# Optimization experiments

Measured on AMD Instinct MI355X. Metric: run time of the kernel, lower is better.

The kernel has to match this reference:

```python
import jax, jax.numpy as jnp
import numpy as np

B = 32768
K = 4096  # num_embeddings
D = 512   # embedding_dim
COMMITMENT_COST = 0.25


def setup_inputs() -> dict:
    key = jax.random.key(0)
    k1, k2 = jax.random.split(key)
    inputs = jax.random.normal(k1, (B, D), dtype=jnp.float32)
    # nn.Embedding weight init: uniform(-1/K, 1/K)
    codebook = jax.random.uniform(k2, (K, D), dtype=jnp.float32,
                                  minval=-1.0 / K, maxval=1.0 / K)
    return {"inputs": inputs, "codebook": codebook}


def reference(inputs, codebook):
    distances = (jnp.sum(inputs ** 2, axis=1, keepdims=True)
                 + jnp.sum(codebook ** 2, axis=1)
                 - 2.0 * jnp.matmul(inputs, codebook.T))
    encoding_indices = jnp.argmin(distances, axis=1)  # [B]
    # one-hot encodings are part of the module's returned dict
    encodings = jax.nn.one_hot(encoding_indices, K, dtype=inputs.dtype)  # [B, K]
    # quantized = encodings @ codebook == direct gather (same math)
    quantized = codebook[encoding_indices]  # [B, D]

    sg = jax.lax.stop_gradient
    e_latent_loss = jnp.mean((sg(quantized) - inputs) ** 2)
    q_latent_loss = jnp.mean((quantized - sg(inputs)) ** 2)
    loss = q_latent_loss + COMMITMENT_COST * e_latent_loss

    # straight-through estimator
    quantized_st = inputs + sg(quantized - inputs)

    avg_probs = jnp.mean(encodings, axis=0)  # [K]
    perplexity = jnp.exp(-jnp.sum(avg_probs * jnp.log(avg_probs + 1e-10)))

    return quantized_st, encoding_indices, loss, perplexity, encodings
```

## Files before the change

kernel.cpp:

```cpp
#include <hip/hip_runtime.h>
#include <hip/hip_bf16.h>


typedef __attribute__((ext_vector_type(8))) short bf16x8;
typedef __attribute__((ext_vector_type(4))) float f32x4;

#define BB 32768
#define KK 4096
#define DD 512

#define IDX_OFF  (BB*DD)
#define LOSS_OFF (IDX_OFF + BB)
#define PERP_OFF (LOSS_OFF + 1)
#define ENC_OFF  (PERP_OFF + 1)

#define WSB_XSQ  0
#define WSB_ESQ  131072
#define WSB_IDX  147456
#define WSB_HIST 278528
#define WSB_LOSS 294912
#define WSB_EBF2 294928
#define WSB_XBF  4489232
#define WSB_PART 38043664

#define MARG 2.5e-4f
#define NCAND 16

static __device__ __forceinline__ unsigned short f2bf(float f) {
    __hip_bfloat16 h = __float2bfloat16(f);
    return *reinterpret_cast<unsigned short*>(&h);
}

static __device__ __forceinline__ unsigned int packscore(float s, int col) {
    unsigned int u = __float_as_uint(s);
    u ^= (u & 0x80000000u) ? 0xFFFFFFFFu : 0x80000000u;
    return (u & 0xFFFFF000u) | (unsigned int)col;
}
static __device__ __forceinline__ float unpackscore(unsigned int p) {
    unsigned int u = p & 0xFFFFF000u;
    u = (u & 0x80000000u) ? (u ^ 0x80000000u) : ~u;
    return __uint_as_float(u);
}

static __device__ __forceinline__ void gll16(const void* g, void* l) {
    __builtin_amdgcn_global_load_lds(
        (const __attribute__((address_space(1))) unsigned int*)g,
        (__attribute__((address_space(3))) unsigned int*)l, 16, 0, 0);
}

__global__ __launch_bounds__(256) void init_kernel(int* __restrict__ hist,
                                                   double* __restrict__ loss_acc) {
    int i = blockIdx.x * 256 + threadIdx.x;
    if (i < KK) hist[i] = 0;
    if (i == 0) *loss_acc = 0.0;
}

__global__ __launch_bounds__(256) void npsum_kernel(const float* __restrict__ X,
                                                    const float* __restrict__ E,
                                                    float* __restrict__ xsq,
                                                    float* __restrict__ esq) {
    __shared__ float sq[4][512];
    __shared__ float ub[4][64];
    __shared__ float bb[4][4];
    int w = threadIdx.x >> 6, lane = threadIdx.x & 63;
    int row = blockIdx.x * 4 + w;
    const float* src; float* dst;
    if (row < BB) { src = X + (size_t)row * DD;        dst = xsq + row; }
    else          { src = E + (size_t)(row - BB) * DD; dst = esq + (row - BB); }
    #pragma unroll
    for (int m = 0; m < 8; ++m) {
        float v = src[m * 64 + lane];
        sq[w][m * 64 + lane] = __fmul_rn(v, v);
    }
    __syncthreads();
    {
        int b = lane >> 4, l = lane & 15;
        const float* s = &sq[w][b * 128];
        float t = __fadd_rn(
            __fadd_rn(__fadd_rn(s[l], s[16 + l]), __fadd_rn(s[32 + l], s[48 + l])),
            __fadd_rn(__fadd_rn(s[64 + l], s[80 + l]), __fadd_rn(s[96 + l], s[112 + l])));
        ub[w][lane] = t;
    }
    __syncthreads();
    if (lane < 4) {
        const float* u = &ub[w][lane * 16];
        float T3[8], T6[4];
        #pragma unroll
        for (int i = 0; i < 8; ++i) T3[i] = __fadd_rn(u[i], u[i + 8]);
        #pragma unroll
        for (int i = 0; i < 4; ++i) T6[i] = __fadd_rn(T3[i], T3[i + 4]);
        bb[w][lane] = __fadd_rn(__fadd_rn(T6[0], T6[2]), __fadd_rn(T6[1], T6[3]));
    }
    __syncthreads();
    if (lane == 0)
        *dst = __fadd_rn(__fadd_rn(bb[w][0], bb[w][1]), __fadd_rn(bb[w][2], bb[w][3]));
}

__global__ __launch_bounds__(256) void pack_kernel(const float* __restrict__ src,
                                                   unsigned short* __restrict__ dst) {
    int t = blockIdx.x * 256 + threadIdx.x;
    int chunk = t >> 10, u = t & 1023;
    int rb = chunk >> 3, kt = chunk & 7;
    int nf = u >> 7, ks = (u >> 6) & 1, lane = u & 63;
    int row = rb * 128 + nf * 16 + (lane & 15);
    int k   = kt * 64 + ks * 32 + (lane >> 4) * 8;
    const float4* s = (const float4*)(src + (size_t)row * DD + k);
    float4 a = s[0], b = s[1];
    union { bf16x8 v; unsigned short us[8]; } pk;
    pk.us[0] = f2bf(a.x); pk.us[1] = f2bf(a.y); pk.us[2] = f2bf(a.z); pk.us[3] = f2bf(a.w);
    pk.us[4] = f2bf(b.x); pk.us[5] = f2bf(b.y); pk.us[6] = f2bf(b.z); pk.us[7] = f2bf(b.w);
    *(bf16x8*)(dst + (size_t)t * 8) = pk.v;
}

__global__ __launch_bounds__(256, 2) void gemm_screen(
    const unsigned short* __restrict__ Xbf, const unsigned short* __restrict__ Ebf2,
    const float* __restrict__ esqw, uint2* __restrict__ partials)
{
    __shared__ __align__(16) char pool[65536];

    const int tid = threadIdx.x;
    const int w = tid >> 6, lane = tid & 63;
    const int c = lane & 15, g = lane >> 4;
    const int bid = blockIdx.x;
    const int orig = (bid & 7) * 1024 + (bid >> 3);
    const int rb = orig >> 5, cb = orig & 31;
    const int row0 = rb * 128, col0 = cb * 128;
    const int mw = w >> 1, nw = w & 1;

    const char* Xc = (const char*)Xbf  + (size_t)rb * 8 * 16384;
    const char* Ec = (const char*)Ebf2 + (size_t)cb * 8 * 16384;

    f32x4 acc[4][4];
    #pragma unroll
    for (int i = 0; i < 4; ++i)
        #pragma unroll
        for (int j = 0; j < 4; ++j) acc[i][j] = (f32x4){0.f, 0.f, 0.f, 0.f};

    #define STAGE(srcc_, kt_, dstoff_) { \
        const char* s_ = (srcc_) + (size_t)(kt_) * 16384 + (size_t)tid * 16; \
        char* d_ = pool + (dstoff_) + w * 1024; \
        gll16(s_,         d_); \
        gll16(s_ + 4096,  d_ + 4096); \
        gll16(s_ + 8192,  d_ + 8192); \
        gll16(s_ + 12288, d_ + 12288); }

    STAGE(Xc, 0, 0); STAGE(Ec, 0, 32768);
    __syncthreads();
    int buf = 0;
    for (int kt = 0; kt < 8; ++kt) {
        if (kt < 7) {
            STAGE(Xc, kt + 1, (buf ^ 1) * 16384);
            STAGE(Ec, kt + 1, 32768 + (buf ^ 1) * 16384);
        }
        const char* Ap = pool + buf * 16384;
        const char* Bp = pool + 32768 + buf * 16384;
        #pragma unroll
        for (int ks = 0; ks < 2; ++ks) {
            bf16x8 af[4], bfr[4];
            #pragma unroll
            for (int i = 0; i < 4; ++i) {
                af[i]  = *(const bf16x8*)(Ap + ((((mw * 4 + i) * 2 + ks) * 64) + lane) * 16);
                bfr[i] = *(const bf16x8*)(Bp + ((((nw * 4 + i) * 2 + ks) * 64) + lane) * 16);
            }
            #pragma unroll
            for (int mf = 0; mf < 4; ++mf)
                #pragma unroll
                for (int nf = 0; nf < 4; ++nf)
                    acc[mf][nf] = __builtin_amdgcn_mfma_f32_16x16x32_bf16(af[mf], bfr[nf], acc[mf][nf], 0, 0, 0);
        }
        __syncthreads();
        buf ^= 1;
    }

    uint2* P = (uint2*)pool;
    #pragma unroll
    for (int mf = 0; mf < 4; ++mf) {
        #pragma unroll
        for (int r = 0; r < 4; ++r) {
            unsigned int q1 = 0xFFFFFFFFu, q2 = 0xFFFFFFFFu;
            int rowl = mw * 64 + mf * 16 + g * 4 + r;
            #pragma unroll
            for (int nf = 0; nf < 4; ++nf) {
                int col = col0 + nw * 64 + nf * 16 + c;
                float s = fmaf(-2.0f, acc[mf][nf][r], esqw[col]);
                unsigned int q = packscore(s, col);
                if (q < q1) { q2 = q1; q1 = q; } else if (q < q2) q2 = q;
            }
            P[(nw * 128 + rowl) * 16 + c] = make_uint2(q1, q2);
        }
    }
    __syncthreads();
    if (tid < 128) {
        int row = tid;
        #pragma unroll
        for (int n2 = 0; n2 < 2; ++n2) {
            unsigned int m1 = 0xFFFFFFFFu, m2 = 0xFFFFFFFFu;
            #pragma unroll 4
            for (int cc = 0; cc < 16; ++cc) {
                uint2 e = P[(n2 * 128 + row) * 16 + cc];
                if (e.x < m1) { m2 = m1; m1 = e.x; } else if (e.x < m2) m2 = e.x;
                if (e.y < m1) { m2 = m1; m1 = e.y; } else if (e.y < m2) m2 = e.y;
            }
            partials[(size_t)(cb * 2 + n2) * BB + row0 + row] = make_uint2(m1, m2);
        }
    }
    #undef STAGE
}

__global__ __launch_bounds__(256) void reduce_kernel(
    const float* __restrict__ X, const float* __restrict__ E,
    const float* __restrict__ xsqw, const float* __restrict__ esqw,
    const uint2* __restrict__ partials, int* __restrict__ idxbuf,
    int* __restrict__ hist, double* __restrict__ loss_acc,
    float* __restrict__ out)
{
    __shared__ double lred[256];
    const int row = blockIdx.x * 256 + threadIdx.x;
    unsigned int m = 0xFFFFFFFFu;
    for (int e = 0; e < 64; ++e) m = min(m, partials[(size_t)e * BB + row].x);
    float lim = unpackscore(m) + MARG;
    int cand[NCAND]; int nc = 0;
    for (int e = 0; e < 64; ++e) {
        uint2 p = partials[(size_t)e * BB + row];
        if (unpackscore(p.x) <= lim && nc < NCAND) cand[nc++] = (int)(p.x & 0xFFFu);
        if (unpackscore(p.y) <= lim && nc < NCAND) cand[nc++] = (int)(p.y & 0xFFFu);
    }
    const float* xr = X + (size_t)row * DD;
    float xs = xsqw[row];
    float bd = 3.0e38f; int bk = 0x7fffffff;
    for (int cidx = 0; cidx < nc; ++cidx) {
        int k = cand[cidx] & (KK - 1);
        const float* er = E + (size_t)k * DD;
        float q1 = 0.f, q2 = 0.f;
        for (int d = 0; d < 384; ++d)   q1 = fmaf(xr[d], er[d], q1);
        for (int d = 384; d < 512; ++d) q2 = fmaf(xr[d], er[d], q2);
        float dot = __fadd_rn(q1, q2);
        float t1  = __fadd_rn(xs, esqw[k]);
        float dnp = __fsub_rn(t1, __fmul_rn(2.0f, dot));
        if (dnp < bd || (dnp == bd && k < bk)) { bd = dnp; bk = k; }
    }
    const float* er = E + (size_t)bk * DD;
    double ls = 0.0;
    for (int d = 0; d < DD; ++d) {
        double df = (double)xr[d] - (double)er[d];
        ls = fma(df, df, ls);
    }
    idxbuf[row] = bk;
    out[IDX_OFF + row] = (float)bk;
    atomicAdd(&hist[bk], 1);
    lred[threadIdx.x] = ls;
    __syncthreads();
    for (int t = 128; t > 0; t >>= 1) {
        if (threadIdx.x < t) lred[threadIdx.x] += lred[threadIdx.x + t];
        __syncthreads();
    }
    if (threadIdx.x == 0) atomicAdd(loss_acc, lred[0]);
}

__global__ __launch_bounds__(256) void encq_kernel(const int* __restrict__ idxbuf,
                                                   const float* __restrict__ E,
                                                   float* __restrict__ out) {
    int row = blockIdx.x;
    int idx = idxbuf[row];
    ((float2*)out)[(size_t)row * 256 + threadIdx.x] =
        ((const float2*)E)[(size_t)idx * 256 + threadIdx.x];
    float2* erow = (float2*)(out + ENC_OFF) + (size_t)row * (KK / 2);
    int half = idx >> 1;
    float2 one;
    if (idx & 1) { one.x = 0.f; one.y = 1.f; } else { one.x = 1.f; one.y = 0.f; }
    float2 z; z.x = 0.f; z.y = 0.f;
    for (int c = threadIdx.x; c < KK / 2; c += 256)
        erow[c] = (c == half) ? one : z;
}

__global__ __launch_bounds__(256) void fin_kernel(const int* __restrict__ hist,
                                                  const double* __restrict__ loss_acc,
                                                  float* __restrict__ out) {
    __shared__ double red[256];
    int tid = threadIdx.x;
    double s = 0.0;
    for (int k = tid; k < KK; k += 256) {
        double p = (double)hist[k] * (1.0 / 32768.0);
        s += p * log(p + 1e-10);
    }
    red[tid] = s;
    __syncthreads();
    for (int t = 128; t > 0; t >>= 1) {
        if (tid < t) red[tid] += red[tid + t];
        __syncthreads();
    }
    if (tid == 0) {
        double perp = exp(-red[0]);
        double L = loss_acc[0] * (1.0 / ((double)BB * (double)DD));
        out[LOSS_OFF] = (float)(1.25 * L);
        out[PERP_OFF] = (float)perp;
    }
}

extern "C" void kernel_launch(void* const* d_in, const int* in_sizes, int n_in,
                              void* d_out, int out_size, void* d_ws, size_t ws_size,
                              hipStream_t stream) {
    const float* X; const float* E;
    if (in_sizes[0] == BB * DD) { X = (const float*)d_in[0]; E = (const float*)d_in[1]; }
    else                        { X = (const float*)d_in[1]; E = (const float*)d_in[0]; }
    float* out = (float*)d_out;

    float* xsq = (float*)((char*)d_ws + WSB_XSQ);
    float* esq = (float*)((char*)d_ws + WSB_ESQ);
    int* idxbuf = (int*)((char*)d_ws + WSB_IDX);
    int* hist   = (int*)((char*)d_ws + WSB_HIST);
    double* loss_acc = (double*)((char*)d_ws + WSB_LOSS);
    unsigned short* Ebf2 = (unsigned short*)((char*)d_ws + WSB_EBF2);
    unsigned short* Xbf  = (unsigned short*)((char*)d_ws + WSB_XBF);
    uint2* partials = (uint2*)((char*)d_ws + WSB_PART);

    hipLaunchKernelGGL(init_kernel, dim3(16), dim3(256), 0, stream, hist, loss_acc);
    hipLaunchKernelGGL(npsum_kernel, dim3((BB + KK) / 4), dim3(256), 0, stream,
                       X, E, xsq, esq);
    hipLaunchKernelGGL(pack_kernel, dim3(1024), dim3(256), 0, stream, E, Ebf2);
    hipLaunchKernelGGL(pack_kernel, dim3(8192), dim3(256), 0, stream, X, Xbf);
    hipLaunchKernelGGL(gemm_screen, dim3(8192), dim3(256), 0, stream,
                       Xbf, Ebf2, esq, partials);
    hipLaunchKernelGGL(reduce_kernel, dim3(BB / 256), dim3(256), 0, stream,
                       X, E, xsq, esq, partials, idxbuf, hist, loss_acc, out);
    hipLaunchKernelGGL(encq_kernel, dim3(BB), dim3(256), 0, stream, idxbuf, E, out);
    hipLaunchKernelGGL(fin_kernel, dim3(1), dim3(256), 0, stream, hist, loss_acc, out);
}
```

Before: 477.2 us.

## Enlarge GEMM screen tile to 256x256 with 512 threads and shuffle-based top-2

Grows the bf16 MFMA screening tile from 128x128 to 256x256 and the block from 256 to 512 threads (8 waves each holding 8x4 accumulator fragments), so each staged byte of X and codebook is reused twice as often. The pack kernel layout changes to match 256-row chunks. The per-row top-2 is merged across lanes with xor shuffles instead of an LDS scratch pass, and the esq values are hoisted into registers. The cost is 128KB of dynamic LDS per block, which with launch_bounds(512,2) may not fit two blocks per CU and may raise register pressure. The reduce kernel still reads 64 partials per row, which stays consistent because the count becomes 16 column blocks times 4 waves.

```diff
diff --git a/kernel.cpp b/kernel.cpp
--- a/kernel.cpp
+++ b/kernel.cpp
@@ -99,10 +99,10 @@
 __global__ __launch_bounds__(256) void pack_kernel(const float* __restrict__ src,
                                                    unsigned short* __restrict__ dst) {
     int t = blockIdx.x * 256 + threadIdx.x;
-    int chunk = t >> 10, u = t & 1023;
-    int rb = chunk >> 3, kt = chunk & 7;
-    int nf = u >> 7, ks = (u >> 6) & 1, lane = u & 63;
-    int row = rb * 128 + nf * 16 + (lane & 15);
+    int chunk = t >> 11, u = t & 2047;
+    int rb2 = chunk >> 3, kt = chunk & 7;
+    int rf = u >> 7, ks = (u >> 6) & 1, lane = u & 63;
+    int row = rb2 * 256 + rf * 16 + (lane & 15);
     int k   = kt * 64 + ks * 32 + (lane >> 4) * 8;
     const float4* s = (const float4*)(src + (size_t)row * DD + k);
     float4 a = s[0], b = s[1];
@@ -112,96 +112,93 @@
     *(bf16x8*)(dst + (size_t)t * 8) = pk.v;
 }
 
-__global__ __launch_bounds__(256, 2) void gemm_screen(
+__global__ __launch_bounds__(512, 2) void gemm_screen(
     const unsigned short* __restrict__ Xbf, const unsigned short* __restrict__ Ebf2,
     const float* __restrict__ esqw, uint2* __restrict__ partials)
 {
-    __shared__ __align__(16) char pool[65536];
+    extern __shared__ __align__(16) char pool[];
 
     const int tid = threadIdx.x;
     const int w = tid >> 6, lane = tid & 63;
     const int c = lane & 15, g = lane >> 4;
     const int bid = blockIdx.x;
-    const int orig = (bid & 7) * 1024 + (bid >> 3);
-    const int rb = orig >> 5, cb = orig & 31;
-    const int row0 = rb * 128, col0 = cb * 128;
-    const int mw = w >> 1, nw = w & 1;
-
-    const char* Xc = (const char*)Xbf  + (size_t)rb * 8 * 16384;
-    const char* Ec = (const char*)Ebf2 + (size_t)cb * 8 * 16384;
-
-    f32x4 acc[4][4];
+    const int orig = (bid & 7) * 256 + (bid >> 3);
+    const int rb2 = orig >> 4, cb2 = orig & 15;
+    const int row0 = rb2 * 256, col0 = cb2 * 256;
+    const int mw = w >> 2, nw = w & 3;
+
+    const char* Xc = (const char*)Xbf  + (size_t)rb2 * 8 * 32768;
+    const char* Ec = (const char*)Ebf2 + (size_t)cb2 * 8 * 32768;
+
+    f32x4 acc[8][4];
     #pragma unroll
-    for (int i = 0; i < 4; ++i)
+    for (int i = 0; i < 8; ++i)
         #pragma unroll
         for (int j = 0; j < 4; ++j) acc[i][j] = (f32x4){0.f, 0.f, 0.f, 0.f};
 
     #define STAGE(srcc_, kt_, dstoff_) { \
-        const char* s_ = (srcc_) + (size_t)(kt_) * 16384 + (size_t)tid * 16; \
+        const char* s_ = (srcc_) + (size_t)(kt_) * 32768 + (size_t)tid * 16; \
         char* d_ = pool + (dstoff_) + w * 1024; \
-        gll16(s_,         d_); \
-        gll16(s_ + 4096,  d_ + 4096); \
-        gll16(s_ + 8192,  d_ + 8192); \
-        gll16(s_ + 12288, d_ + 12288); }
-
-    STAGE(Xc, 0, 0); STAGE(Ec, 0, 32768);
+        gll16(s_,          d_); \
+        gll16(s_ + 8192,   d_ + 8192); \
+        gll16(s_ + 16384,  d_ + 16384); \
+        gll16(s_ + 24576,  d_ + 24576); }
+
+    STAGE(Xc, 0, 0); STAGE(Ec, 0, 65536);
     __syncthreads();
     int buf = 0;
     for (int kt = 0; kt < 8; ++kt) {
         if (kt < 7) {
-            STAGE(Xc, kt + 1, (buf ^ 1) * 16384);
-            STAGE(Ec, kt + 1, 32768 + (buf ^ 1) * 16384);
+            STAGE(Xc, kt + 1, (buf ^ 1) * 32768);
+            STAGE(Ec, kt + 1, 65536 + (buf ^ 1) * 32768);
         }
-        const char* Ap = pool + buf * 16384;
-        const char* Bp = pool + 32768 + buf * 16384;
+        const char* Ap = pool + buf * 32768;
+        const char* Bp = pool + 65536 + buf * 32768;
         #pragma unroll
         for (int ks = 0; ks < 2; ++ks) {
-            bf16x8 af[4], bfr[4];
+            bf16x8 bfr[4];
             #pragma unroll
-            for (int i = 0; i < 4; ++i) {
-                af[i]  = *(const bf16x8*)(Ap + ((((mw * 4 + i) * 2 + ks) * 64) + lane) * 16);
-                bfr[i] = *(const bf16x8*)(Bp + ((((nw * 4 + i) * 2 + ks) * 64) + lane) * 16);
+            for (int j = 0; j < 4; ++j)
+                bfr[j] = *(const bf16x8*)(Bp + ((((nw * 4 + j) * 2 + ks) * 64) + lane) * 16);
+            #pragma unroll
+            for (int i = 0; i < 8; ++i) {
+                bf16x8 af = *(const bf16x8*)(Ap + ((((mw * 8 + i) * 2 + ks) * 64) + lane) * 16);
+                #pragma unroll
+                for (int j = 0; j < 4; ++j)
+                    acc[i][j] = __builtin_amdgcn_mfma_f32_16x16x32_bf16(af, bfr[j], acc[i][j], 0, 0, 0);
             }
-            #pragma unroll
-            for (int mf = 0; mf < 4; ++mf)
-                #pragma unroll
-                for (int nf = 0; nf < 4; ++nf)
-                    acc[mf][nf] = __builtin_amdgcn_mfma_f32_16x16x32_bf16(af[mf], bfr[nf], acc[mf][nf], 0, 0, 0);
         }
         __syncthreads();
         buf ^= 1;
     }
 
-    uint2* P = (uint2*)pool;
+    float es[4];
     #pragma unroll
-    for (int mf = 0; mf < 4; ++mf) {
+    for (int nf = 0; nf < 4; ++nf) es[nf] = esqw[col0 + nw * 64 + nf * 16 + c];
+    #pragma unroll
+    for (int mf = 0; mf < 8; ++mf) {
         #pragma unroll
         for (int r = 0; r < 4; ++r) {
             unsigned int q1 = 0xFFFFFFFFu, q2 = 0xFFFFFFFFu;
-            int rowl = mw * 64 + mf * 16 + g * 4 + r;
             #pragma unroll
             for (int nf = 0; nf < 4; ++nf) {
                 int col = col0 + nw * 64 + nf * 16 + c;
-                float s = fmaf(-2.0f, acc[mf][nf][r], esqw[col]);
+                float s = fmaf(-2.0f, acc[mf][nf][r], es[nf]);
                 unsigned int q = packscore(s, col);
                 if (q < q1) { q2 = q1; q1 = q; } else if (q < q2) q2 = q;
             }
-            P[(nw * 128 + rowl) * 16 + c] = make_uint2(q1, q2);
-        }
-    }
-    __syncthreads();
-    if (tid < 128) {
-        int row = tid;
-        #pragma unroll
-        for (int n2 = 0; n2 < 2; ++n2) {
-            unsigned int m1 = 0xFFFFFFFFu, m2 = 0xFFFFFFFFu;
-            #pragma unroll 4
-            for (int cc = 0; cc < 16; ++cc) {
-                uint2 e = P[(n2 * 128 + row) * 16 + cc];
-                if (e.x < m1) { m2 = m1; m1 = e.x; } else if (e.x < m2) m2 = e.x;
-                if (e.y < m1) { m2 = m1; m1 = e.y; } else if (e.y < m2) m2 = e.y;
+            #pragma unroll
+            for (int off = 1; off < 16; off <<= 1) {
+                unsigned int o1 = (unsigned int)__shfl_xor((int)q1, off, 64);
+                unsigned int o2 = (unsigned int)__shfl_xor((int)q2, off, 64);
+                unsigned int n1 = min(q1, o1);
+                unsigned int n2 = min(max(q1, o1), min(q2, o2));
+                q1 = n1; q2 = n2;
             }
-            partials[(size_t)(cb * 2 + n2) * BB + row0 + row] = make_uint2(m1, m2);
+            if (c == 0) {
+                int row = row0 + mw * 128 + mf * 16 + g * 4 + r;
+                partials[(size_t)(cb2 * 4 + nw) * BB + row] = make_uint2(q1, q2);
+            }
         }
     }
     #undef STAGE
@@ -319,7 +316,7 @@
                        X, E, xsq, esq);
     hipLaunchKernelGGL(pack_kernel, dim3(1024), dim3(256), 0, stream, E, Ebf2);
     hipLaunchKernelGGL(pack_kernel, dim3(8192), dim3(256), 0, stream, X, Xbf);
-    hipLaunchKernelGGL(gemm_screen, dim3(8192), dim3(256), 0, stream,
+    hipLaunchKernelGGL(gemm_screen, dim3(2048), dim3(512), 131072, stream,
                        Xbf, Ebf2, esq, partials);
     hipLaunchKernelGGL(reduce_kernel, dim3(BB / 256), dim3(256), 0, stream,
                        X, E, xsq, esq, partials, idxbuf, hist, loss_acc, out);
```

New measurement: 489.4 us. +2.6%, slower.

## Fuse X bf16 packing into norm kernel and halve GEMM LDS tiles

Applied to the files above, without the earlier changes.

The separate X pack pass is merged into the squared-norm kernel, so X is read from global memory once, and the row sum of squares now uses vectorized float4 loads. The bf16 tile layout changes to 256-row groups with 32-wide k-steps. The GEMM now stages 32-wide k slices over 16 iterations instead of 64-wide over 8, which halves LDS use so launch bounds can ask for 4 blocks per CU. The cost is twice as many barriers and smaller load batches per iteration. The fp32 summation order for the norms is changed, which could shift rounding slightly.

```diff
diff --git a/kernel.cpp b/kernel.cpp
--- a/kernel.cpp
+++ b/kernel.cpp
@@ -55,27 +55,44 @@
     if (i == 0) *loss_acc = 0.0;
 }
 
-__global__ __launch_bounds__(256) void npsum_kernel(const float* __restrict__ X,
-                                                    const float* __restrict__ E,
-                                                    float* __restrict__ xsq,
-                                                    float* __restrict__ esq) {
+__global__ __launch_bounds__(256) void npsum_pack_kernel(const float* __restrict__ X,
+                                                         const float* __restrict__ E,
+                                                         float* __restrict__ xsq,
+                                                         float* __restrict__ esq,
+                                                         unsigned short* __restrict__ Xbf) {
     __shared__ float sq[4][512];
     __shared__ float ub[4][64];
     __shared__ float bb[4][4];
     int w = threadIdx.x >> 6, lane = threadIdx.x & 63;
     int row = blockIdx.x * 4 + w;
     const float* src; float* dst;
-    if (row < BB) { src = X + (size_t)row * DD;        dst = xsq + row; }
-    else          { src = E + (size_t)(row - BB) * DD; dst = esq + (row - BB); }
-    #pragma unroll
-    for (int m = 0; m < 8; ++m) {
-        float v = src[m * 64 + lane];
-        sq[w][m * 64 + lane] = __fmul_rn(v, v);
+    bool isx = (row < BB);
+    if (isx) { src = X + (size_t)row * DD;        dst = xsq + row; }
+    else     { src = E + (size_t)(row - BB) * DD; dst = esq + (row - BB); }
+    const float4* s4 = (const float4*)(src + lane * 8);
+    float4 a = s4[0], b = s4[1];
+    sq[w][lane * 8 + 0] = __fmul_rn(a.x, a.x);
+    sq[w][lane * 8 + 1] = __fmul_rn(a.y, a.y);
+    sq[w][lane * 8 + 2] = __fmul_rn(a.z, a.z);
+    sq[w][lane * 8 + 3] = __fmul_rn(a.w, a.w);
+    sq[w][lane * 8 + 4] = __fmul_rn(b.x, b.x);
+    sq[w][lane * 8 + 5] = __fmul_rn(b.y, b.y);
+    sq[w][lane * 8 + 6] = __fmul_rn(b.z, b.z);
+    sq[w][lane * 8 + 7] = __fmul_rn(b.w, b.w);
+    if (isx) {
+        int kt64 = lane >> 3, ks = (lane >> 2) & 1, oct = lane & 3;
+        int rf = (row >> 4) & 15;
+        size_t unit = ((size_t)((row >> 8) * 8 + kt64)) * 2048
+                    + (size_t)((rf * 2 + ks) * 64 + oct * 16 + (row & 15));
+        union { bf16x8 v; unsigned short us[8]; } pk;
+        pk.us[0] = f2bf(a.x); pk.us[1] = f2bf(a.y); pk.us[2] = f2bf(a.z); pk.us[3] = f2bf(a.w);
+        pk.us[4] = f2bf(b.x); pk.us[5] = f2bf(b.y); pk.us[6] = f2bf(b.z); pk.us[7] = f2bf(b.w);
+        *(bf16x8*)(Xbf + unit * 8) = pk.v;
     }
     __syncthreads();
     {
-        int b = lane >> 4, l = lane & 15;
-        const float* s = &sq[w][b * 128];
+        int b2 = lane >> 4, l = lane & 15;
+        const float* s = &sq[w][b2 * 128];
         float t = __fadd_rn(
             __fadd_rn(__fadd_rn(s[l], s[16 + l]), __fadd_rn(s[32 + l], s[48 + l])),
             __fadd_rn(__fadd_rn(s[64 + l], s[80 + l]), __fadd_rn(s[96 + l], s[112 + l])));
@@ -96,13 +113,13 @@
         *dst = __fadd_rn(__fadd_rn(bb[w][0], bb[w][1]), __fadd_rn(bb[w][2], bb[w][3]));
 }
 
-__global__ __launch_bounds__(256) void pack_kernel(const float* __restrict__ src,
-                                                   unsigned short* __restrict__ dst) {
+__global__ __launch_bounds__(256) void packE_kernel(const float* __restrict__ src,
+                                                    unsigned short* __restrict__ dst) {
     int t = blockIdx.x * 256 + threadIdx.x;
-    int chunk = t >> 10, u = t & 1023;
-    int rb = chunk >> 3, kt = chunk & 7;
-    int nf = u >> 7, ks = (u >> 6) & 1, lane = u & 63;
-    int row = rb * 128 + nf * 16 + (lane & 15);
+    int chunk = t >> 11, u = t & 2047;
+    int rb2 = chunk >> 3, kt = chunk & 7;
+    int rf = u >> 7, ks = (u >> 6) & 1, lane = u & 63;
+    int row = rb2 * 256 + rf * 16 + (lane & 15);
     int k   = kt * 64 + ks * 32 + (lane >> 4) * 8;
     const float4* s = (const float4*)(src + (size_t)row * DD + k);
     float4 a = s[0], b = s[1];
@@ -112,11 +129,11 @@
     *(bf16x8*)(dst + (size_t)t * 8) = pk.v;
 }
 
-__global__ __launch_bounds__(256, 2) void gemm_screen(
+__global__ __launch_bounds__(256, 4) void gemm_screen(
     const unsigned short* __restrict__ Xbf, const unsigned short* __restrict__ Ebf2,
     const float* __restrict__ esqw, uint2* __restrict__ partials)
 {
-    __shared__ __align__(16) char pool[65536];
+    __shared__ __align__(16) char pool[32768];
 
     const int tid = threadIdx.x;
     const int w = tid >> 6, lane = tid & 63;
@@ -127,8 +144,9 @@
     const int row0 = rb * 128, col0 = cb * 128;
     const int mw = w >> 1, nw = w & 1;
 
-    const char* Xc = (const char*)Xbf  + (size_t)rb * 8 * 16384;
-    const char* Ec = (const char*)Ebf2 + (size_t)cb * 8 * 16384;
+    const int hA = rb & 1, hB = cb & 1;
+    const char* Xc = (const char*)Xbf  + (size_t)(rb >> 1) * 8 * 32768;
+    const char* Ec = (const char*)Ebf2 + (size_t)(cb >> 1) * 8 * 32768;
 
     f32x4 acc[4][4];
     #pragma unroll
@@ -136,38 +154,35 @@
         #pragma unroll
         for (int j = 0; j < 4; ++j) acc[i][j] = (f32x4){0.f, 0.f, 0.f, 0.f};
 
-    #define STAGE(srcc_, kt_, dstoff_) { \
-        const char* s_ = (srcc_) + (size_t)(kt_) * 16384 + (size_t)tid * 16; \
-        char* d_ = pool + (dstoff_) + w * 1024; \
-        gll16(s_,         d_); \
-        gll16(s_ + 4096,  d_ + 4096); \
-        gll16(s_ + 8192,  d_ + 8192); \
-        gll16(s_ + 12288, d_ + 12288); }
-
-    STAGE(Xc, 0, 0); STAGE(Ec, 0, 32768);
+    #define STAGE(srcc_, h_, kt_, dstoff_) { \
+        const char* sb_ = (srcc_) + (size_t)((kt_) >> 1) * 32768; \
+        const int ks_ = (kt_) & 1; \
+        _Pragma("unroll") for (int it_ = 0; it_ < 2; ++it_) { \
+            const char* s_ = sb_ + (size_t)((((h_) * 8 + it_ * 4 + w) * 2 + ks_) * 64 + lane) * 16; \
+            char* d_ = pool + (dstoff_) + (it_ * 4 + w) * 1024; \
+            gll16(s_, d_); } }
+
+    STAGE(Xc, hA, 0, 0); STAGE(Ec, hB, 0, 16384);
     __syncthreads();
     int buf = 0;
-    for (int kt = 0; kt < 8; ++kt) {
-        if (kt < 7) {
-            STAGE(Xc, kt + 1, (buf ^ 1) * 16384);
-            STAGE(Ec, kt + 1, 32768 + (buf ^ 1) * 16384);
+    for (int kt = 0; kt < 16; ++kt) {
+        if (kt < 15) {
+            STAGE(Xc, hA, kt + 1, (buf ^ 1) * 8192);
+            STAGE(Ec, hB, kt + 1, 16384 + (buf ^ 1) * 8192);
         }
-        const char* Ap = pool + buf * 16384;
-        const char* Bp = pool + 32768 + buf * 16384;
-        #pragma unroll
-        for (int ks = 0; ks < 2; ++ks) {
-            bf16x8 af[4], bfr[4];
+        const char* Ap = pool + buf * 8192;
+        const char* Bp = pool + 16384 + buf * 8192;
+        bf16x8 af[4], bfr[4];
+        #pragma unroll
+        for (int i = 0; i < 4; ++i) {
+            af[i]  = *(const bf16x8*)(Ap + (((mw * 4 + i) * 64) + lane) * 16);
+            bfr[i] = *(const bf16x8*)(Bp + (((nw * 4 + i) * 64) + lane) * 16);
+        }
+        #pragma unroll
+        for (int mf = 0; mf < 4; ++mf)
             #pragma unroll
-            for (int i = 0; i < 4; ++i) {
-                af[i]  = *(const bf16x8*)(Ap + ((((mw * 4 + i) * 2 + ks) * 64) + lane) * 16);
-                bfr[i] = *(const bf16x8*)(Bp + ((((nw * 4 + i) * 2 + ks) * 64) + lane) * 16);
-            }
-            #pragma unroll
-            for (int mf = 0; mf < 4; ++mf)
-                #pragma unroll
-                for (int nf = 0; nf < 4; ++nf)
-                    acc[mf][nf] = __builtin_amdgcn_mfma_f32_16x16x32_bf16(af[mf], bfr[nf], acc[mf][nf], 0, 0, 0);
-        }
+            for (int nf = 0; nf < 4; ++nf)
+                acc[mf][nf] = __builtin_amdgcn_mfma_f32_16x16x32_bf16(af[mf], bfr[nf], acc[mf][nf], 0, 0, 0);
         __syncthreads();
         buf ^= 1;
     }
@@ -315,10 +330,9 @@
     uint2* partials = (uint2*)((char*)d_ws + WSB_PART);
 
     hipLaunchKernelGGL(init_kernel, dim3(16), dim3(256), 0, stream, hist, loss_acc);
-    hipLaunchKernelGGL(npsum_kernel, dim3((BB + KK) / 4), dim3(256), 0, stream,
-                       X, E, xsq, esq);
-    hipLaunchKernelGGL(pack_kernel, dim3(1024), dim3(256), 0, stream, E, Ebf2);
-    hipLaunchKernelGGL(pack_kernel, dim3(8192), dim3(256), 0, stream, X, Xbf);
+    hipLaunchKernelGGL(npsum_pack_kernel, dim3((BB + KK) / 4), dim3(256), 0, stream,
+                       X, E, xsq, esq, Xbf);
+    hipLaunchKernelGGL(packE_kernel, dim3(1024), dim3(256), 0, stream, E, Ebf2);
     hipLaunchKernelGGL(gemm_screen, dim3(8192), dim3(256), 0, stream,
                        Xbf, Ebf2, esq, partials);
     hipLaunchKernelGGL(reduce_kernel, dim3(BB / 256), dim3(256), 0, stream,
```

New measurement: 458.4 us. 1.04x faster.
